# Performance work log

Measured on AMD Instinct MI355X. Metric: run time of the kernel, lower is better.

## Reference

```python
import jax, jax.numpy as jnp
import numpy as np

K_SIZE = 5  # kernel_size


def _patches(f, k):
    # f: (b, c, h, w) -> (b, c, k*k, h, w), matching torch.nn.Unfold ordering
    # (patch positions row-major (kh, kw) per channel), padding = k//2, stride 1.
    p = k // 2
    b, c, h, w = f.shape
    fp = jnp.pad(f, ((0, 0), (0, 0), (p, p), (p, p)))
    slices = [fp[:, :, i:i + h, j:j + w] for i in range(k) for j in range(k)]
    return jnp.stack(slices, axis=2)


def _conv1x1(w, b, f):
    # w: (out, in), b: (out,), f: (b, in, h, w)
    return jnp.einsum('oc,bchw->bohw', w, f) + b[None, :, None, None]


def setup_inputs() -> dict:
    key = jax.random.key(0)
    ks = jax.random.split(key, 8)
    B, XC, YC, FT, H, W = 4, 64, 64, 64, 128, 128
    x = jax.random.normal(ks[0], (B, XC, H, W), dtype=jnp.float32)
    y = jax.random.normal(ks[1], (B, YC, H, W), dtype=jnp.float32)
    sx = 1.0 / np.sqrt(XC)
    sy = 1.0 / np.sqrt(YC)
    sf = 1.0 / np.sqrt(FT)
    wx = jax.random.uniform(ks[2], (FT, XC), jnp.float32, -sx, sx)
    bx = jax.random.uniform(ks[3], (FT,), jnp.float32, -sx, sx)
    wy = jax.random.uniform(ks[4], (FT, YC), jnp.float32, -sy, sy)
    by = jax.random.uniform(ks[5], (FT,), jnp.float32, -sy, sy)
    wo = jax.random.uniform(ks[6], (XC, FT), jnp.float32, -sf, sf)
    bo = jax.random.uniform(ks[7], (XC,), jnp.float32, -sf, sf)
    return {"x": x, "y": y, "wx": wx, "bx": bx, "wy": wy, "by": by, "wo": wo, "bo": bo}


def reference(x, y, wx, bx, wy, by, wo, bo):
    k = K_SIZE
    q = _conv1x1(wy, by, y)            # (b, feat, h, w): Q (the q axis of size 1 is squeezed)
    Kp = _patches(q, k)                # (b, feat, k^2, h, w): unfold(conv_y(y))
    v = _conv1x1(wx, bx, x)            # (b, feat, h, w)
    Vp = _patches(v, k)                # (b, feat, k^2, h, w): unfold(conv_x(x))
    A = jnp.einsum('bckhw,bchw->bkhw', Kp, q)   # scores over k^2 neighbors
    A = jax.nn.softmax(A, axis=1)               # softmax over dim=1 (k^2)
    out = jnp.einsum('bkhw,bckhw->bchw', A, Vp)  # aggregate values
    out = _conv1x1(wo, bo, out)
    return out + x
```

## Files before the change

### kernel.cpp

```cpp
#include <hip/hip_runtime.h>

#define HH   128
#define WW   128
#define HW   (HH * WW)
#define CC   64
#define TILE 8
#define HALO 12
#define NHP  (HALO * HALO)

typedef unsigned int uint32;
typedef _Float16 h2   __attribute__((ext_vector_type(2)));
typedef __fp16   h2b  __attribute__((ext_vector_type(2)));
typedef _Float16 h8   __attribute__((ext_vector_type(8)));
typedef float    f32x4 __attribute__((ext_vector_type(4)));

__device__ __forceinline__ uint32 pkrtz(float a, float b) {
    h2b r = __builtin_amdgcn_cvt_pkrtz(a, b);
    return __builtin_bit_cast(uint32, r);
}
__device__ __forceinline__ float dot2(uint32 a, uint32 b, float c) {
#if __has_builtin(__builtin_amdgcn_fdot2)
    return __builtin_amdgcn_fdot2(__builtin_bit_cast(h2b, a),
                                  __builtin_bit_cast(h2b, b), c, false);
#else
    h2 x = __builtin_bit_cast(h2, a), y = __builtin_bit_cast(h2, b);
    return c + (float)x.x * (float)y.x + (float)x.y * (float)y.y;
#endif
}
__device__ __forceinline__ f32x4 mfma16(uint4 a, uint4 b, f32x4 c) {
    return __builtin_amdgcn_mfma_f32_16x16x32_f16(
        __builtin_bit_cast(h8, a), __builtin_bit_cast(h8, b), c, 0, 0, 0);
}
__device__ __forceinline__ uint4 pack_w8(const float* __restrict__ w) {
    const float4 lo = *(const float4*)w;
    const float4 hi = *(const float4*)(w + 4);
    uint4 r;
    r.x = pkrtz(lo.x, lo.y); r.y = pkrtz(lo.z, lo.w);
    r.z = pkrtz(hi.x, hi.y); r.w = pkrtz(hi.z, hi.w);
    return r;
}

__global__ __launch_bounds__(256, 4)
void fused_attn(const float* __restrict__ x, const float* __restrict__ y,
                const float* __restrict__ wx, const float* __restrict__ bx,
                const float* __restrict__ wy, const float* __restrict__ by,
                const float* __restrict__ wo, const float* __restrict__ bo,
                float* __restrict__ out)
{
    __shared__ uint32 qh[NHP * 32];
    __shared__ uint32 vh[NHP * 32];

    const int t   = threadIdx.x;
    const int b   = blockIdx.z;
    const int ty0 = blockIdx.y * TILE;
    const int tx0 = blockIdx.x * TILE;

    for (int i = t; i < NHP * 8; i += 256) {
        const int c   = i / NHP;
        const int pix = i - c * NHP;
        const int hy  = pix / HALO, hx = pix - hy * HALO;
        int gy = ty0 + hy - 2, gx = tx0 + hx - 2;
        const bool ok = ((unsigned)gy < HH) & ((unsigned)gx < WW);
        if (!ok) { gy = 0; gx = 0; }
        const size_t base = (size_t)b * CC * HW + (size_t)(c * 8) * HW
                          + (size_t)gy * WW + gx;
        float yv[8], xv[8];
        #pragma unroll
        for (int j = 0; j < 8; ++j) {
            yv[j] = y[base + (size_t)j * HW];
            xv[j] = x[base + (size_t)j * HW];
        }
        uint4 yq, xq;
        yq.x = pkrtz(yv[0], yv[1]); yq.y = pkrtz(yv[2], yv[3]);
        yq.z = pkrtz(yv[4], yv[5]); yq.w = pkrtz(yv[6], yv[7]);
        xq.x = pkrtz(xv[0], xv[1]); xq.y = pkrtz(xv[2], xv[3]);
        xq.z = pkrtz(xv[4], xv[5]); xq.w = pkrtz(xv[6], xv[7]);
        const int w0 = (c ^ (pix & 7)) * 4;
        *(uint4*)&qh[pix * 32 + w0] = yq;
        *(uint4*)&vh[pix * 32 + w0] = xq;
    }
    __syncthreads();

    const int wv = t >> 6;
    const int ln = t & 63;
    const int lm = ln & 15;
    const int qd = ln >> 4;

    {
        const uint4 a0 = pack_w8(wy + (wv * 16 + lm) * CC + qd * 8);
        const uint4 a1 = pack_w8(wy + (wv * 16 + lm) * CC + qd * 8 + 32);
        f32x4 acc[9];
        #pragma unroll
        for (int nt = 0; nt < 9; ++nt) {
            const int px = nt * 16 + lm, sw = px & 7;
            const uint4 b0 = *(const uint4*)&qh[px * 32 + ((qd    ) ^ sw) * 4];
            const uint4 b1 = *(const uint4*)&qh[px * 32 + ((qd + 4) ^ sw) * 4];
            f32x4 a = {0.f, 0.f, 0.f, 0.f};
            a = mfma16(a0, b0, a);
            a = mfma16(a1, b1, a);
            acc[nt] = a;
        }
        __syncthreads();
        const float4 bq = *(const float4*)(by + wv * 16 + qd * 4);
        const int chunk = wv * 2 + (qd >> 1);
        #pragma unroll
        for (int nt = 0; nt < 9; ++nt) {
            const int px = nt * 16 + lm;
            const int hy = px / HALO, hx = px - hy * HALO;
            const int gy = ty0 + hy - 2, gx = tx0 + hx - 2;
            uint2 wp = {0u, 0u};
            if (((unsigned)gy < HH) & ((unsigned)gx < WW)) {
                wp.x = pkrtz(acc[nt].x + bq.x, acc[nt].y + bq.y);
                wp.y = pkrtz(acc[nt].z + bq.z, acc[nt].w + bq.w);
            }
            *(uint2*)&qh[px * 32 + (chunk ^ (px & 7)) * 4 + (qd & 1) * 2] = wp;
        }
    }

    {
        const uint4 a0 = pack_w8(wx + (wv * 16 + lm) * CC + qd * 8);
        const uint4 a1 = pack_w8(wx + (wv * 16 + lm) * CC + qd * 8 + 32);
        f32x4 acc[9];
        #pragma unroll
        for (int nt = 0; nt < 9; ++nt) {
            const int px = nt * 16 + lm, sw = px & 7;
            const uint4 b0 = *(const uint4*)&vh[px * 32 + ((qd    ) ^ sw) * 4];
            const uint4 b1 = *(const uint4*)&vh[px * 32 + ((qd + 4) ^ sw) * 4];
            f32x4 a = {0.f, 0.f, 0.f, 0.f};
            a = mfma16(a0, b0, a);
            a = mfma16(a1, b1, a);
            acc[nt] = a;
        }
        __syncthreads();
        const float4 bq = *(const float4*)(bx + wv * 16 + qd * 4);
        const int chunk = wv * 2 + (qd >> 1);
        #pragma unroll
        for (int nt = 0; nt < 9; ++nt) {
            const int px = nt * 16 + lm;
            const int hy = px / HALO, hx = px - hy * HALO;
            const int gy = ty0 + hy - 2, gx = tx0 + hx - 2;
            uint2 wp = {0u, 0u};
            if (((unsigned)gy < HH) & ((unsigned)gx < WW)) {
                wp.x = pkrtz(acc[nt].x + bq.x, acc[nt].y + bq.y);
                wp.y = pkrtz(acc[nt].z + bq.z, acc[nt].w + bq.w);
            }
            *(uint2*)&vh[px * 32 + (chunk ^ (px & 7)) * 4 + (qd & 1) * 2] = wp;
        }
    }
    __syncthreads();

    const int p    = t >> 2, sub = t & 3;
    const int py   = p >> 3, px8 = p & 7;
    const int crow = (py + 2) * HALO + (px8 + 2);

    uint32 qc[8];
    {
        const int c0 = ((2 * sub) ^ (crow & 7)) * 4;
        const int c1 = ((2 * sub + 1) ^ (crow & 7)) * 4;
        *(uint4*)&qc[0] = *(const uint4*)&qh[crow * 32 + c0];
        *(uint4*)&qc[4] = *(const uint4*)&qh[crow * 32 + c1];
    }

    float sc[25];
    #pragma unroll
    for (int dy = 0; dy < 5; ++dy)
        #pragma unroll
        for (int dx = 0; dx < 5; ++dx) {
            const int nrow = (py + dy) * HALO + (px8 + dx);
            const int c0 = ((2 * sub) ^ (nrow & 7)) * 4;
            const int c1 = ((2 * sub + 1) ^ (nrow & 7)) * 4;
            const uint4 r0 = *(const uint4*)&qh[nrow * 32 + c0];
            const uint4 r1 = *(const uint4*)&qh[nrow * 32 + c1];
            float s = 0.f;
            s = dot2(qc[0], r0.x, s); s = dot2(qc[1], r0.y, s);
            s = dot2(qc[2], r0.z, s); s = dot2(qc[3], r0.w, s);
            s = dot2(qc[4], r1.x, s); s = dot2(qc[5], r1.y, s);
            s = dot2(qc[6], r1.z, s); s = dot2(qc[7], r1.w, s);
            s += __shfl_xor(s, 1);
            s += __shfl_xor(s, 2);
            sc[dy * 5 + dx] = s;
        }

    float mx = sc[0];
    #pragma unroll
    for (int k = 1; k < 25; ++k) mx = fmaxf(mx, sc[k]);
    float sum = 0.f;
    #pragma unroll
    for (int k = 0; k < 25; ++k) { sc[k] = __expf(sc[k] - mx); sum += sc[k]; }
    const float inv = 1.f / sum;

    h2 ag[8];
    #pragma unroll
    for (int k = 0; k < 8; ++k) ag[k] = (h2)(_Float16)0;
    #pragma unroll
    for (int dy = 0; dy < 5; ++dy)
        #pragma unroll
        for (int dx = 0; dx < 5; ++dx) {
            const int nrow = (py + dy) * HALO + (px8 + dx);
            const int c0 = ((2 * sub) ^ (nrow & 7)) * 4;
            const int c1 = ((2 * sub + 1) ^ (nrow & 7)) * 4;
            const uint4 r0 = *(const uint4*)&vh[nrow * 32 + c0];
            const uint4 r1 = *(const uint4*)&vh[nrow * 32 + c1];
            const _Float16 af = (_Float16)(sc[dy * 5 + dx] * inv);
            const h2 a2 = {af, af};
            ag[0] += a2 * __builtin_bit_cast(h2, r0.x);
            ag[1] += a2 * __builtin_bit_cast(h2, r0.y);
            ag[2] += a2 * __builtin_bit_cast(h2, r0.z);
            ag[3] += a2 * __builtin_bit_cast(h2, r0.w);
            ag[4] += a2 * __builtin_bit_cast(h2, r1.x);
            ag[5] += a2 * __builtin_bit_cast(h2, r1.y);
            ag[6] += a2 * __builtin_bit_cast(h2, r1.z);
            ag[7] += a2 * __builtin_bit_cast(h2, r1.w);
        }

    __syncthreads();
    {
        const int c0 = ((2 * sub) ^ (p & 7)) * 4;
        const int c1 = ((2 * sub + 1) ^ (p & 7)) * 4;
        uint4 w0, w1;
        w0.x = __builtin_bit_cast(uint32, ag[0]); w0.y = __builtin_bit_cast(uint32, ag[1]);
        w0.z = __builtin_bit_cast(uint32, ag[2]); w0.w = __builtin_bit_cast(uint32, ag[3]);
        w1.x = __builtin_bit_cast(uint32, ag[4]); w1.y = __builtin_bit_cast(uint32, ag[5]);
        w1.z = __builtin_bit_cast(uint32, ag[6]); w1.w = __builtin_bit_cast(uint32, ag[7]);
        *(uint4*)&qh[p * 32 + c0] = w0;
        *(uint4*)&qh[p * 32 + c1] = w1;
    }
    __syncthreads();

    {
        const uint4 a0 = pack_w8(wo + (wv * 16 + lm) * CC + qd * 8);
        const uint4 a1 = pack_w8(wo + (wv * 16 + lm) * CC + qd * 8 + 32);
        const float4 bq = *(const float4*)(bo + wv * 16 + qd * 4);
        #pragma unroll
        for (int nt = 0; nt < 4; ++nt) {
            const int px = nt * 16 + lm, sw = px & 7;
            const uint4 b0 = *(const uint4*)&qh[px * 32 + ((qd    ) ^ sw) * 4];
            const uint4 b1 = *(const uint4*)&qh[px * 32 + ((qd + 4) ^ sw) * 4];
            f32x4 a = {0.f, 0.f, 0.f, 0.f};
            a = mfma16(a0, b0, a);
            a = mfma16(a1, b1, a);
            const int gh = ty0 + (px >> 3), gw = tx0 + (px & 7);
            const float av4[4] = {a.x + bq.x, a.y + bq.y, a.z + bq.z, a.w + bq.w};
            #pragma unroll
            for (int r = 0; r < 4; ++r) {
                const int oc = wv * 16 + qd * 4 + r;
                const size_t ad = (size_t)(b * CC + oc) * HW + (size_t)gh * WW + gw;
                out[ad] = av4[r] + x[ad];
            }
        }
    }
}

extern "C" void kernel_launch(void* const* d_in, const int* in_sizes, int n_in,
                              void* d_out, int out_size, void* d_ws, size_t ws_size,
                              hipStream_t stream) {
    const float* x  = (const float*)d_in[0];
    const float* y  = (const float*)d_in[1];
    const float* wx = (const float*)d_in[2];
    const float* bx = (const float*)d_in[3];
    const float* wy = (const float*)d_in[4];
    const float* by = (const float*)d_in[5];
    const float* wo = (const float*)d_in[6];
    const float* bo = (const float*)d_in[7];
    float* out = (float*)d_out;
    (void)d_ws; (void)ws_size;

    dim3 grid(WW / TILE, HH / TILE, 4);
    fused_attn<<<grid, 256, 0, stream>>>(x, y, wx, bx, wy, by, wo, bo, out);
}
```

Measured before the change: 136.7 us.

## Merge Q/V projections, reuse staged fp16 x for residual, remap grid to XCDs

Runs both 1x1 projection MFMA loops in one pass with a single barrier instead of two. The residual add now reads the fp16 copy of x already staged in LDS instead of re-reading fp32 x from global memory. The launch becomes a 1D grid whose block index is decoded so each XCD handles a contiguous half-image of one batch, aiming for better L2 locality. The residual is now fp16-rounded, which reduces accuracy, and more accumulators stay live at once, raising register pressure.

```diff
diff --git a/kernel.cpp b/kernel.cpp
--- a/kernel.cpp
+++ b/kernel.cpp
@@ -47,13 +47,18 @@
                 const float* __restrict__ wo, const float* __restrict__ bo,
                 float* __restrict__ out)
 {
-    __shared__ uint32 qh[NHP * 32];
-    __shared__ uint32 vh[NHP * 32];
-
-    const int t   = threadIdx.x;
-    const int b   = blockIdx.z;
-    const int ty0 = blockIdx.y * TILE;
-    const int tx0 = blockIdx.x * TILE;
+    __shared__ uint32 Ah[NHP * 32];
+    __shared__ uint32 Bh[NHP * 32];
+
+    const int lin  = blockIdx.x;
+    const int xcd  = lin & 7;
+    const int rr   = lin >> 3;
+    const int b    = xcd >> 1;
+    const int half = xcd & 1;
+    const int ty0  = (((rr >> 4) + half * 8)) * TILE;
+    const int tx0  = (rr & 15) * TILE;
+
+    const int t = threadIdx.x;
 
     for (int i = t; i < NHP * 8; i += 256) {
         const int c   = i / NHP;
@@ -76,8 +81,8 @@
         xq.x = pkrtz(xv[0], xv[1]); xq.y = pkrtz(xv[2], xv[3]);
         xq.z = pkrtz(xv[4], xv[5]); xq.w = pkrtz(xv[6], xv[7]);
         const int w0 = (c ^ (pix & 7)) * 4;
-        *(uint4*)&qh[pix * 32 + w0] = yq;
-        *(uint4*)&vh[pix * 32 + w0] = xq;
+        *(uint4*)&Ah[pix * 32 + w0] = yq;
+        *(uint4*)&Bh[pix * 32 + w0] = xq;
     }
     __syncthreads();
 
@@ -86,65 +91,55 @@
     const int lm = ln & 15;
     const int qd = ln >> 4;
 
-    {
-        const uint4 a0 = pack_w8(wy + (wv * 16 + lm) * CC + qd * 8);
-        const uint4 a1 = pack_w8(wy + (wv * 16 + lm) * CC + qd * 8 + 32);
-        f32x4 acc[9];
+    f32x4 accq[9], accv[9];
+    uint2 xres[4];
+    {
+        const uint4 aq0 = pack_w8(wy + (wv * 16 + lm) * CC + qd * 8);
+        const uint4 aq1 = pack_w8(wy + (wv * 16 + lm) * CC + qd * 8 + 32);
+        const uint4 av0 = pack_w8(wx + (wv * 16 + lm) * CC + qd * 8);
+        const uint4 av1 = pack_w8(wx + (wv * 16 + lm) * CC + qd * 8 + 32);
         #pragma unroll
         for (int nt = 0; nt < 9; ++nt) {
             const int px = nt * 16 + lm, sw = px & 7;
-            const uint4 b0 = *(const uint4*)&qh[px * 32 + ((qd    ) ^ sw) * 4];
-            const uint4 b1 = *(const uint4*)&qh[px * 32 + ((qd + 4) ^ sw) * 4];
+            const uint4 b0 = *(const uint4*)&Ah[px * 32 + ((qd    ) ^ sw) * 4];
+            const uint4 b1 = *(const uint4*)&Ah[px * 32 + ((qd + 4) ^ sw) * 4];
             f32x4 a = {0.f, 0.f, 0.f, 0.f};
-            a = mfma16(a0, b0, a);
-            a = mfma16(a1, b1, a);
-            acc[nt] = a;
-        }
-        __syncthreads();
+            a = mfma16(aq0, b0, a); a = mfma16(aq1, b1, a); accq[nt] = a;
+            const uint4 c0 = *(const uint4*)&Bh[px * 32 + ((qd    ) ^ sw) * 4];
+            const uint4 c1 = *(const uint4*)&Bh[px * 32 + ((qd + 4) ^ sw) * 4];
+            f32x4 v = {0.f, 0.f, 0.f, 0.f};
+            v = mfma16(av0, c0, v); v = mfma16(av1, c1, v); accv[nt] = v;
+        }
+        #pragma unroll
+        for (int nt = 0; nt < 4; ++nt) {
+            const int px = nt * 16 + lm;
+            const int hpix = ((px >> 3) + 2) * HALO + (px & 7) + 2;
+            const int chunk = wv * 2 + (qd >> 1);
+            xres[nt] = *(const uint2*)
+                &Bh[hpix * 32 + (chunk ^ (hpix & 7)) * 4 + (qd & 1) * 2];
+        }
+    }
+    __syncthreads();
+
+    {
         const float4 bq = *(const float4*)(by + wv * 16 + qd * 4);
+        const float4 bv = *(const float4*)(bx + wv * 16 + qd * 4);
         const int chunk = wv * 2 + (qd >> 1);
         #pragma unroll
         for (int nt = 0; nt < 9; ++nt) {
             const int px = nt * 16 + lm;
             const int hy = px / HALO, hx = px - hy * HALO;
             const int gy = ty0 + hy - 2, gx = tx0 + hx - 2;
-            uint2 wp = {0u, 0u};
+            uint2 wq = {0u, 0u}, wvv = {0u, 0u};
             if (((unsigned)gy < HH) & ((unsigned)gx < WW)) {
-                wp.x = pkrtz(acc[nt].x + bq.x, acc[nt].y + bq.y);
-                wp.y = pkrtz(acc[nt].z + bq.z, acc[nt].w + bq.w);
+                wq.x  = pkrtz(accq[nt].x + bq.x, accq[nt].y + bq.y);
+                wq.y  = pkrtz(accq[nt].z + bq.z, accq[nt].w + bq.w);
+                wvv.x = pkrtz(accv[nt].x + bv.x, accv[nt].y + bv.y);
+                wvv.y = pkrtz(accv[nt].z + bv.z, accv[nt].w + bv.w);
             }
-            *(uint2*)&qh[px * 32 + (chunk ^ (px & 7)) * 4 + (qd & 1) * 2] = wp;
-        }
-    }
-
-    {
-        const uint4 a0 = pack_w8(wx + (wv * 16 + lm) * CC + qd * 8);
-        const uint4 a1 = pack_w8(wx + (wv * 16 + lm) * CC + qd * 8 + 32);
-        f32x4 acc[9];
-        #pragma unroll
-        for (int nt = 0; nt < 9; ++nt) {
-            const int px = nt * 16 + lm, sw = px & 7;
-            const uint4 b0 = *(const uint4*)&vh[px * 32 + ((qd    ) ^ sw) * 4];
-            const uint4 b1 = *(const uint4*)&vh[px * 32 + ((qd + 4) ^ sw) * 4];
-            f32x4 a = {0.f, 0.f, 0.f, 0.f};
-            a = mfma16(a0, b0, a);
-            a = mfma16(a1, b1, a);
-            acc[nt] = a;
-        }
-        __syncthreads();
-        const float4 bq = *(const float4*)(bx + wv * 16 + qd * 4);
-        const int chunk = wv * 2 + (qd >> 1);
-        #pragma unroll
-        for (int nt = 0; nt < 9; ++nt) {
-            const int px = nt * 16 + lm;
-            const int hy = px / HALO, hx = px - hy * HALO;
-            const int gy = ty0 + hy - 2, gx = tx0 + hx - 2;
-            uint2 wp = {0u, 0u};
-            if (((unsigned)gy < HH) & ((unsigned)gx < WW)) {
-                wp.x = pkrtz(acc[nt].x + bq.x, acc[nt].y + bq.y);
-                wp.y = pkrtz(acc[nt].z + bq.z, acc[nt].w + bq.w);
-            }
-            *(uint2*)&vh[px * 32 + (chunk ^ (px & 7)) * 4 + (qd & 1) * 2] = wp;
+            const int off = px * 32 + (chunk ^ (px & 7)) * 4 + (qd & 1) * 2;
+            *(uint2*)&Ah[off] = wq;
+            *(uint2*)&Bh[off] = wvv;
         }
     }
     __syncthreads();
@@ -157,8 +152,8 @@
     {
         const int c0 = ((2 * sub) ^ (crow & 7)) * 4;
         const int c1 = ((2 * sub + 1) ^ (crow & 7)) * 4;
-        *(uint4*)&qc[0] = *(const uint4*)&qh[crow * 32 + c0];
-        *(uint4*)&qc[4] = *(const uint4*)&qh[crow * 32 + c1];
+        *(uint4*)&qc[0] = *(const uint4*)&Ah[crow * 32 + c0];
+        *(uint4*)&qc[4] = *(const uint4*)&Ah[crow * 32 + c1];
     }
 
     float sc[25];
@@ -169,8 +164,8 @@
             const int nrow = (py + dy) * HALO + (px8 + dx);
             const int c0 = ((2 * sub) ^ (nrow & 7)) * 4;
             const int c1 = ((2 * sub + 1) ^ (nrow & 7)) * 4;
-            const uint4 r0 = *(const uint4*)&qh[nrow * 32 + c0];
-            const uint4 r1 = *(const uint4*)&qh[nrow * 32 + c1];
+            const uint4 r0 = *(const uint4*)&Ah[nrow * 32 + c0];
+            const uint4 r1 = *(const uint4*)&Ah[nrow * 32 + c1];
             float s = 0.f;
             s = dot2(qc[0], r0.x, s); s = dot2(qc[1], r0.y, s);
             s = dot2(qc[2], r0.z, s); s = dot2(qc[3], r0.w, s);
@@ -199,8 +194,8 @@
             const int nrow = (py + dy) * HALO + (px8 + dx);
             const int c0 = ((2 * sub) ^ (nrow & 7)) * 4;
             const int c1 = ((2 * sub + 1) ^ (nrow & 7)) * 4;
-            const uint4 r0 = *(const uint4*)&vh[nrow * 32 + c0];
-            const uint4 r1 = *(const uint4*)&vh[nrow * 32 + c1];
+            const uint4 r0 = *(const uint4*)&Bh[nrow * 32 + c0];
+            const uint4 r1 = *(const uint4*)&Bh[nrow * 32 + c1];
             const _Float16 af = (_Float16)(sc[dy * 5 + dx] * inv);
             const h2 a2 = {af, af};
             ag[0] += a2 * __builtin_bit_cast(h2, r0.x);
@@ -222,8 +217,8 @@
         w0.z = __builtin_bit_cast(uint32, ag[2]); w0.w = __builtin_bit_cast(uint32, ag[3]);
         w1.x = __builtin_bit_cast(uint32, ag[4]); w1.y = __builtin_bit_cast(uint32, ag[5]);
         w1.z = __builtin_bit_cast(uint32, ag[6]); w1.w = __builtin_bit_cast(uint32, ag[7]);
-        *(uint4*)&qh[p * 32 + c0] = w0;
-        *(uint4*)&qh[p * 32 + c1] = w1;
+        *(uint4*)&Ah[p * 32 + c0] = w0;
+        *(uint4*)&Ah[p * 32 + c1] = w1;
     }
     __syncthreads();
 
@@ -234,18 +229,22 @@
         #pragma unroll
         for (int nt = 0; nt < 4; ++nt) {
             const int px = nt * 16 + lm, sw = px & 7;
-            const uint4 b0 = *(const uint4*)&qh[px * 32 + ((qd    ) ^ sw) * 4];
-            const uint4 b1 = *(const uint4*)&qh[px * 32 + ((qd + 4) ^ sw) * 4];
+            const uint4 b0 = *(const uint4*)&Ah[px * 32 + ((qd    ) ^ sw) * 4];
+            const uint4 b1 = *(const uint4*)&Ah[px * 32 + ((qd + 4) ^ sw) * 4];
             f32x4 a = {0.f, 0.f, 0.f, 0.f};
             a = mfma16(a0, b0, a);
             a = mfma16(a1, b1, a);
             const int gh = ty0 + (px >> 3), gw = tx0 + (px & 7);
+            const h2 xp0 = __builtin_bit_cast(h2, xres[nt].x);
+            const h2 xp1 = __builtin_bit_cast(h2, xres[nt].y);
+            const float rv[4] = {(float)xp0.x, (float)xp0.y,
+                                 (float)xp1.x, (float)xp1.y};
             const float av4[4] = {a.x + bq.x, a.y + bq.y, a.z + bq.z, a.w + bq.w};
             #pragma unroll
             for (int r = 0; r < 4; ++r) {
                 const int oc = wv * 16 + qd * 4 + r;
                 const size_t ad = (size_t)(b * CC + oc) * HW + (size_t)gh * WW + gw;
-                out[ad] = av4[r] + x[ad];
+                out[ad] = av4[r] + rv[r];
             }
         }
     }
@@ -265,6 +264,5 @@
     float* out = (float*)d_out;
     (void)d_ws; (void)ws_size;
 
-    dim3 grid(WW / TILE, HH / TILE, 4);
-    fused_attn<<<grid, 256, 0, stream>>>(x, y, wx, bx, wy, by, wo, bo, out);
-}
+    fused_attn<<<dim3(1024), 256, 0, stream>>>(x, y, wx, bx, wy, by, wo, bo, out);
+}
```

After: 115.9 us. 15.2% less time.
